# Optimization experiments

Measured on AMD Instinct MI355X. Metric: run time of the kernel, lower is better.

Reference implementation:

```python
import jax, jax.numpy as jnp
import numpy as np

H = 8        # num_heads
KNN = 16     # k nearest neighbors
D = 256      # input_dim
LN_EPS = 1e-5


def _make_params(key, D):
    ks = jax.random.split(key, 10)
    def lin(k, din, dout):
        k1, k2 = jax.random.split(k)
        lim = 1.0 / np.sqrt(din)
        W = jax.random.uniform(k1, (din, dout), jnp.float32, -lim, lim)
        b = jax.random.uniform(k2, (dout,), jnp.float32, -lim, lim)
        return W, b
    Wq, bq = lin(ks[0], D, D)
    Wk, bk = lin(ks[1], D, D)
    Wv, bv = lin(ks[2], D, D)
    Wo1, bo1 = lin(ks[3], D, D)
    ln_g = jnp.ones((D,), jnp.float32)
    ln_b = jnp.zeros((D,), jnp.float32)
    Wo2, bo2 = lin(ks[4], D, D)
    return dict(Wq=Wq, bq=bq, Wk=Wk, bk=bk, Wv=Wv, bv=bv,
                Wo1=Wo1, bo1=bo1, ln_g=ln_g, ln_b=ln_b, Wo2=Wo2, bo2=bo2)


def setup_inputs() -> dict:
    key = jax.random.key(0)
    k1, k2, k3, k4, k5 = jax.random.split(key, 5)
    B, N, M = 2, 2048, 4096
    inp = {
        "src": jax.random.normal(k1, (B, N, 3), jnp.float32),
        "tgt": jax.random.normal(k2, (B, M, 3), jnp.float32),
        "src_fea": jax.random.normal(k3, (B, N, D), jnp.float32),
        "tgt_fea": jax.random.normal(k4, (B, M, D), jnp.float32),
    }
    inp.update(_make_params(k5, D))
    return inp


def _cdist(x, y):
    # Euclidean distance [B,N,M], matching torch.cdist(p=2)
    x2 = jnp.sum(x * x, axis=-1, keepdims=True)          # [B,N,1]
    y2 = jnp.sum(y * y, axis=-1, keepdims=True)          # [B,M,1]
    sq = x2 + jnp.swapaxes(y2, -1, -2) - 2.0 * jnp.einsum('bnc,bmc->bnm', x, y)
    return jnp.sqrt(jnp.maximum(sq, 0.0))


def _layernorm(x, g, b):
    mu = jnp.mean(x, axis=-1, keepdims=True)
    var = jnp.mean((x - mu) ** 2, axis=-1, keepdims=True)
    return (x - mu) * jax.lax.rsqrt(var + LN_EPS) * g + b


def reference(src, tgt, src_fea, tgt_fea, Wq, bq, Wk, bk, Wv, bv,
              Wo1, bo1, ln_g, ln_b, Wo2, bo2):
    B, N, Dm = src_fea.shape
    M = tgt.shape[1]
    dk = Dm // H
    scale = dk ** (-0.5)

    # kNN mask: distances [B,N,M], topk smallest -> boolean mask
    dist = _cdist(src, tgt)
    _, knn_idx = jax.lax.top_k(-dist, KNN)               # [B,N,KNN]
    bi = jnp.arange(B)[:, None, None]
    ni = jnp.arange(N)[None, :, None]
    mask = jnp.zeros((B, N, M), bool).at[bi, ni, knn_idx].set(True)

    # projections -> [B,H,*,dk]
    Q = (src_fea @ Wq + bq).reshape(B, N, H, dk).transpose(0, 2, 1, 3)
    K = (tgt_fea @ Wk + bk).reshape(B, M, H, dk).transpose(0, 2, 1, 3)
    V = (tgt_fea @ Wv + bv).reshape(B, M, H, dk).transpose(0, 2, 1, 3)

    scores = jnp.einsum('bhnd,bhmd->bhnm', Q, K) * scale
    scores = jnp.where(mask[:, None], scores, -jnp.inf)
    attn = jax.nn.softmax(scores, axis=-1)               # [B,H,N,M]

    out = jnp.einsum('bhnm,bhmd->bhnd', attn, V)
    out = out.transpose(0, 2, 1, 3).reshape(B, N, Dm)

    x = out + src_fea
    h = jax.nn.relu(_layernorm(x @ Wo1 + bo1, ln_g, ln_b))
    updated = h @ Wo2 + bo2

    avg_attn = jnp.mean(attn, axis=1)                    # [B,N,M]
    return updated, avg_attn
```

## Files before the change

kernel.cpp:

```cpp
#include <hip/hip_runtime.h>
#include <math.h>

#define BB 2
#define NN 2048
#define MM 4096
#define DD 256
#define HH 8
#define DK 32
#define KNN 16

typedef __attribute__((ext_vector_type(8))) short short8;
typedef __attribute__((ext_vector_type(4))) float f32x4;
typedef unsigned long long u64;
typedef unsigned short u16;

static __device__ __forceinline__ u16 f2bf(float f) {
    union { float f; unsigned u; } v; v.f = f;
    unsigned r = v.u + 0x7FFF + ((v.u >> 16) & 1);
    return (u16)(r >> 16);
}
static __device__ __forceinline__ float bf2f(u16 u) {
    union { unsigned u; float f; } v; v.u = ((unsigned)u) << 16;
    return v.f;
}

__global__ __launch_bounds__(256)
void wtrans(const float* W0, const float* W1, const float* W2, const float* W3, const float* W4,
            u16* O0, u16* O1, u16* O2, u16* O3, u16* O4)
{
    __shared__ float tile[64][65];
    const int bid = blockIdx.x;
    const int m = bid >> 4, tl = bid & 15;
    const int tr = (tl >> 2) * 64, tc = (tl & 3) * 64;
    const float* W = m == 0 ? W0 : m == 1 ? W1 : m == 2 ? W2 : m == 3 ? W3 : W4;
    u16*        O = m == 0 ? O0 : m == 1 ? O1 : m == 2 ? O2 : m == 3 ? O3 : O4;
    const int c = threadIdx.x & 63, r4 = threadIdx.x >> 6;
    #pragma unroll
    for (int i = 0; i < 16; ++i) {
        const int r = (r4 << 4) + i;
        tile[r][c] = W[(size_t)(tr + r) * 256 + tc + c];
    }
    __syncthreads();
    #pragma unroll
    for (int i = 0; i < 16; ++i) {
        const int cc = (r4 << 4) + i;
        O[(size_t)(tc + cc) * 256 + tr + c] = f2bf(tile[c][cc]);
    }
}

static __device__ __forceinline__ void gemm64_body(
    const float* __restrict__ A, size_t row0, const u16* __restrict__ WT, int col0,
    u16* As, u16* Bs, int t, f32x4 acc[2][2])
{
    const int lane = t & 63, w = t >> 6;
    const int wr = (w >> 1) * 32, wc = (w & 1) * 32;
    for (int k0 = 0; k0 < 256; k0 += 64) {
        #pragma unroll
        for (int e = 0; e < 2; ++e) {
            const int flat = t + (e << 8);
            const int r = flat >> 3, kc = (flat & 7) << 3;
            const int off = ((r << 7) + (kc << 1)) ^ ((r & 7) << 4);
            const float* ap = A + (row0 + r) * 256 + k0 + kc;
            float4 a0 = *(const float4*)ap;
            float4 a1 = *(const float4*)(ap + 4);
            short8 s;
            s[0] = (short)f2bf(a0.x); s[1] = (short)f2bf(a0.y);
            s[2] = (short)f2bf(a0.z); s[3] = (short)f2bf(a0.w);
            s[4] = (short)f2bf(a1.x); s[5] = (short)f2bf(a1.y);
            s[6] = (short)f2bf(a1.z); s[7] = (short)f2bf(a1.w);
            *(short8*)((char*)As + off) = s;
            *(short8*)((char*)Bs + off) = *(const short8*)(WT + (size_t)(col0 + r) * 256 + k0 + kc);
        }
        __syncthreads();
        #pragma unroll
        for (int kk = 0; kk < 64; kk += 32) {
            const int kbo = (kk + ((lane >> 4) << 3)) << 1;
            short8 af[2], bfr[2];
            #pragma unroll
            for (int i = 0; i < 2; ++i) {
                const int ra = wr + (i << 4) + (lane & 15);
                af[i]  = *(const short8*)((const char*)As + (((ra << 7) + kbo) ^ ((ra & 7) << 4)));
                const int rb = wc + (i << 4) + (lane & 15);
                bfr[i] = *(const short8*)((const char*)Bs + (((rb << 7) + kbo) ^ ((rb & 7) << 4)));
            }
            #pragma unroll
            for (int mi = 0; mi < 2; ++mi)
                #pragma unroll
                for (int ni = 0; ni < 2; ++ni)
                    acc[mi][ni] = __builtin_amdgcn_mfma_f32_16x16x32_bf16(af[mi], bfr[ni], acc[mi][ni], 0, 0, 0);
        }
        __syncthreads();
    }
}

__global__ __launch_bounds__(256, 4)
void mega_kernel(const float* __restrict__ src, const float* __restrict__ tgt,
                 int* __restrict__ knn_idx,
                 const float* __restrict__ tgt_fea, const float* __restrict__ src_fea,
                 const u16* __restrict__ WTq, const u16* __restrict__ WTkv,
                 const float* __restrict__ bq, const float* __restrict__ bk,
                 const float* __restrict__ bv,
                 float* __restrict__ Qb, u16* __restrict__ Kbf, u16* __restrict__ Vbf,
                 float* __restrict__ avg)
{
    __shared__ u16 As[64 * 64];
    __shared__ u16 Bs[64 * 64];
    const int bid = blockIdx.x;
    const int t = threadIdx.x;
    const int lane = t & 63;
    const int lid = bid / 11;
    const int role = bid % 11;

    if (role < 4) {
        const int kb = lid * 4 + role;
        const int bn = (kb << 2) + (t >> 6);
        const int b = bn >> 11;
        const float* sp = src + (size_t)bn * 3;
        const float px = sp[0], py = sp[1], pz = sp[2];
        const float x2 = px * px + py * py + pz * pz;
        const float* tb = tgt + (size_t)b * MM * 3;
        unsigned key[64];
        #pragma unroll
        for (int j = 0; j < 64; ++j) {
            const int m = (j << 6) + lane;
            const float tx = tb[m * 3 + 0], ty = tb[m * 3 + 1], tz = tb[m * 3 + 2];
            const float y2 = tx * tx + ty * ty + tz * tz;
            const float dt = px * tx + py * ty + pz * tz;
            float d = (x2 + y2) - 2.0f * dt;
            d = d > 0.f ? d : 0.f;
            const unsigned q20 = (unsigned)fminf(d * 32768.0f, 1048575.0f);
            key[j] = (q20 << 12) | (unsigned)m;
        }
        unsigned last1 = 0;
        unsigned mykey = 0xFFFFFFFFu;
        for (int sel = 0; sel < 20; ++sel) {
            unsigned c0 = ~0u, c1 = ~0u, c2 = ~0u, c3 = ~0u;
            #pragma unroll
            for (int j = 0; j < 64; j += 4) {
                const unsigned u0 = key[j + 0] - last1; c0 = u0 < c0 ? u0 : c0;
                const unsigned u1 = key[j + 1] - last1; c1 = u1 < c1 ? u1 : c1;
                const unsigned u2 = key[j + 2] - last1; c2 = u2 < c2 ? u2 : c2;
                const unsigned u3 = key[j + 3] - last1; c3 = u3 < c3 ? u3 : c3;
            }
            unsigned best = c0 < c1 ? c0 : c1;
            const unsigned bst2 = c2 < c3 ? c2 : c3;
            best = best < bst2 ? best : bst2;
            #pragma unroll
            for (int s = 32; s; s >>= 1) {
                const unsigned o = __shfl_xor(best, s, 64);
                best = o < best ? o : best;
            }
            const unsigned winner = best + last1;
            if (lane == sel) mykey = winner;
            last1 = winner + 1;
        }
        const int midx = (int)(mykey & 0xFFFu);
        u64 ex = ~0ULL;
        if (lane < 20) {
            const float* tp = tb + (size_t)midx * 3;
            const double pxd = px, pyd = py, pzd = pz;
            const double tx = tp[0], ty = tp[1], tz = tp[2];
            const double x2d = pxd * pxd + pyd * pyd + pzd * pzd;
            const double y2d = tx * tx + ty * ty + tz * tz;
            const double dtd = pxd * tx + pyd * ty + pzd * tz;
            double dd = (x2d + y2d) - 2.0 * dtd;
            dd = dd > 0.0 ? dd : 0.0;
            ex = (((u64)__double_as_longlong(dd)) & ~0xFFFULL) | (u64)midx;
        }
        int rank = 0;
        #pragma unroll
        for (int i = 0; i < 20; ++i) {
            const u64 o = __shfl(ex, i, 64);
            rank += (o < ex) ? 1 : 0;
        }
        if (lane < 20 && rank < 16)
            knn_idx[(size_t)bn * KNN + rank] = midx;
        return;
    }

    if (role < 8) {
        const int kvb = lid * 4 + (role - 4);
        const size_t row0 = (size_t)(kvb >> 3) * 64;
        const int col0 = (kvb & 7) * 64;
        f32x4 acc[2][2] = {};
        gemm64_body(tgt_fea, row0, WTkv, col0, As, Bs, t, acc);
        const int w = t >> 6;
        const int wr = (w >> 1) * 32, wc = (w & 1) * 32;
        const bool isv = col0 >= 256;
        u16* ob = isv ? Vbf : Kbf;
        const float* bs = isv ? bv : bk;
        const int cb = (isv ? col0 - 256 : col0) + wc;
        const int cq = lane & 15, rq = (lane >> 4) << 2;
        #pragma unroll
        for (int ni = 0; ni < 2; ++ni) {
            const int c = cb + (ni << 4) + cq;
            const float bval = bs[c];
            #pragma unroll
            for (int mi = 0; mi < 2; ++mi) {
                const size_t r = row0 + wr + (mi << 4) + rq;
                #pragma unroll
                for (int e = 0; e < 4; ++e)
                    ob[(r + e) * 256 + c] = f2bf(acc[mi][ni][e] + bval);
            }
        }
        return;
    }

    if (role == 8) {
        const int qb = lid;
        const size_t row0 = (size_t)(qb >> 2) * 64;
        const int col0 = (qb & 3) * 64;
        f32x4 acc[2][2] = {};
        gemm64_body(src_fea, row0, WTq, col0, As, Bs, t, acc);
        const int w = t >> 6;
        const int wr = (w >> 1) * 32, wc = (w & 1) * 32;
        const int cq = lane & 15, rq = (lane >> 4) << 2;
        #pragma unroll
        for (int ni = 0; ni < 2; ++ni) {
            const int c = col0 + wc + (ni << 4) + cq;
            const float bval = bq[c];
            #pragma unroll
            for (int mi = 0; mi < 2; ++mi) {
                const size_t rbase = (row0 + wr + (mi << 4) + rq) * 256 + c;
                #pragma unroll
                for (int e = 0; e < 4; ++e)
                    Qb[rbase + (size_t)e * 256] = acc[mi][ni][e] + bval;
            }
        }
        return;
    }

    {
        const int zb = lid * 2 + (role - 9);
        f32x4 z = {0.f, 0.f, 0.f, 0.f};
        f32x4* pz = (f32x4*)avg;
        const int base = zb * 256 + t;
        #pragma unroll
        for (int i = 0; i < 32; ++i)
            pz[base + i * 131072] = z;
    }
}

__global__ __launch_bounds__(256)
void attn_kernel(const float* __restrict__ Q, const u16* __restrict__ Kb,
                 const u16* __restrict__ Vb, const int* __restrict__ knn_idx,
                 const float* __restrict__ src_fea,
                 u16* __restrict__ Xb, float* __restrict__ avg_attn)
{
    __shared__ float Kt[KNN][257];
    __shared__ float Vt[KNN][257];
    __shared__ float q[DD];
    __shared__ float sc[HH][KNN];
    __shared__ float pw[HH][KNN];
    __shared__ int   idx[KNN];
    const int bn = blockIdx.x;
    const int b  = bn >> 11;
    const int t  = threadIdx.x;
    if (t < KNN) idx[t] = knn_idx[(size_t)bn * KNN + t];
    q[t] = Q[(size_t)bn * DD + t];
    __syncthreads();
    {
        const int l32 = t & 31, rg = t >> 5;
        #pragma unroll
        for (int rr = 0; rr < 2; ++rr) {
            const int r = (rr << 3) + rg;
            const size_t rowoff = ((size_t)b * MM + idx[r]) * DD + (l32 << 3);
            const short8 kv = *(const short8*)(Kb + rowoff);
            const short8 vv = *(const short8*)(Vb + rowoff);
            #pragma unroll
            for (int e = 0; e < 8; ++e) {
                Kt[r][(l32 << 3) + e] = bf2f((u16)kv[e]);
                Vt[r][(l32 << 3) + e] = bf2f((u16)vv[e]);
            }
        }
    }
    __syncthreads();
    if (t < HH * KNN) {
        int h = t >> 4, k = t & 15;
        float s = 0.f;
        const float* qh = &q[h * DK];
        const float* kh = &Kt[k][h * DK];
        #pragma unroll
        for (int j = 0; j < DK; ++j) s = fmaf(qh[j], kh[j], s);
        sc[h][k] = s * 0.17677669529663688f;
    }
    __syncthreads();
    if (t < HH) {
        float mx = -1e30f;
        #pragma unroll
        for (int k = 0; k < KNN; ++k) mx = fmaxf(mx, sc[t][k]);
        float e[KNN]; float sum = 0.f;
        #pragma unroll
        for (int k = 0; k < KNN; ++k) { e[k] = expf(sc[t][k] - mx); sum += e[k]; }
        float inv = 1.0f / sum;
        #pragma unroll
        for (int k = 0; k < KNN; ++k) pw[t][k] = e[k] * inv;
    }
    __syncthreads();
    if (t < KNN) {
        float a = 0.f;
        #pragma unroll
        for (int h = 0; h < HH; ++h) a += pw[h][t];
        avg_attn[(size_t)bn * MM + idx[t]] = a * (1.0f / HH);
    }
    {
        int h = t >> 5;
        float acc = 0.f;
        #pragma unroll
        for (int k = 0; k < KNN; ++k) acc = fmaf(pw[h][k], Vt[k][t], acc);
        Xb[(size_t)bn * DD + t] = f2bf(acc + src_fea[(size_t)bn * DD + t]);
    }
}

template<int LN>
__global__ __launch_bounds__(256)
void gemm_row256(const u16* __restrict__ A, const u16* __restrict__ WT,
                 const float* __restrict__ bias,
                 const float* __restrict__ g, const float* __restrict__ bvec,
                 u16* __restrict__ outb, float* __restrict__ outf)
{
    __shared__ u16 As[64 * 64];
    __shared__ u16 Bs[256 * 64];
    const int t = threadIdx.x, lane = t & 63, w = t >> 6;
    const size_t row0 = (size_t)blockIdx.x * 64;
    f32x4 acc[4][4] = {};
    for (int k0 = 0; k0 < 256; k0 += 64) {
        #pragma unroll
        for (int e = 0; e < 2; ++e) {
            const int u = t + (e << 8);
            const int r = u >> 3, kc = (u & 7) << 3;
            const int off = ((r << 7) + (kc << 1)) ^ ((r & 7) << 4);
            *(short8*)((char*)As + off) = *(const short8*)(A + (row0 + r) * 256 + k0 + kc);
        }
        #pragma unroll
        for (int e = 0; e < 8; ++e) {
            const int u = t + (e << 8);
            const int r = u >> 3, kc = (u & 7) << 3;
            const int off = ((r << 7) + (kc << 1)) ^ ((r & 7) << 4);
            *(short8*)((char*)Bs + off) = *(const short8*)(WT + (size_t)r * 256 + k0 + kc);
        }
        __syncthreads();
        #pragma unroll
        for (int kk = 0; kk < 64; kk += 32) {
            const int kbo = (kk + ((lane >> 4) << 3)) << 1;
            short8 af[4], bfr[4];
            #pragma unroll
            for (int i = 0; i < 4; ++i) {
                const int ra = (i << 4) + (lane & 15);
                af[i]  = *(const short8*)((const char*)As + (((ra << 7) + kbo) ^ ((ra & 7) << 4)));
                const int rb = (w << 6) + (i << 4) + (lane & 15);
                bfr[i] = *(const short8*)((const char*)Bs + (((rb << 7) + kbo) ^ ((rb & 7) << 4)));
            }
            #pragma unroll
            for (int mi = 0; mi < 4; ++mi)
                #pragma unroll
                for (int ni = 0; ni < 4; ++ni)
                    acc[mi][ni] = __builtin_amdgcn_mfma_f32_16x16x32_bf16(af[mi], bfr[ni], acc[mi][ni], 0, 0, 0);
        }
        __syncthreads();
    }
    const int cq = lane & 15, rq = (lane >> 4) << 2;
    #pragma unroll
    for (int ni = 0; ni < 4; ++ni) {
        const float bval = bias[(w << 6) + (ni << 4) + cq];
        #pragma unroll
        for (int mi = 0; mi < 4; ++mi)
            #pragma unroll
            for (int e = 0; e < 4; ++e)
                acc[mi][ni][e] += bval;
    }
    if (LN) {
        float* ws1 = (float*)As;
        float* ws2 = ws1 + 256;
        float s1v[4][4], s2v[4][4];
        #pragma unroll
        for (int mi = 0; mi < 4; ++mi)
            #pragma unroll
            for (int e = 0; e < 4; ++e) {
                float s1 = 0.f, s2 = 0.f;
                #pragma unroll
                for (int ni = 0; ni < 4; ++ni) { const float y = acc[mi][ni][e]; s1 += y; s2 += y * y; }
                #pragma unroll
                for (int s = 8; s; s >>= 1) { s1 += __shfl_xor(s1, s, 64); s2 += __shfl_xor(s2, s, 64); }
                s1v[mi][e] = s1; s2v[mi][e] = s2;
            }
        if (cq == 0) {
            #pragma unroll
            for (int mi = 0; mi < 4; ++mi)
                #pragma unroll
                for (int e = 0; e < 4; ++e) {
                    const int r = (mi << 4) + rq + e;
                    ws1[(w << 6) + r] = s1v[mi][e];
                    ws2[(w << 6) + r] = s2v[mi][e];
                }
        }
        __syncthreads();
        float g4[4], b4[4];
        #pragma unroll
        for (int ni = 0; ni < 4; ++ni) {
            const int c = (w << 6) + (ni << 4) + cq;
            g4[ni] = g[c]; b4[ni] = bvec[c];
        }
        #pragma unroll
        for (int mi = 0; mi < 4; ++mi)
            #pragma unroll
            for (int e = 0; e < 4; ++e) {
                const int r = (mi << 4) + rq + e;
                const float s1 = ws1[r] + ws1[64 + r] + ws1[128 + r] + ws1[192 + r];
                const float s2 = ws2[r] + ws2[64 + r] + ws2[128 + r] + ws2[192 + r];
                const float mean = s1 * (1.0f / 256.0f);
                const float var = s2 * (1.0f / 256.0f) - mean * mean;
                const float rstd = 1.0f / sqrtf(var + 1e-5f);
                #pragma unroll
                for (int ni = 0; ni < 4; ++ni) {
                    const int c = (w << 6) + (ni << 4) + cq;
                    float y = (acc[mi][ni][e] - mean) * rstd * g4[ni] + b4[ni];
                    outb[(row0 + r) * 256 + c] = f2bf(fmaxf(y, 0.0f));
                }
            }
    } else {
        #pragma unroll
        for (int ni = 0; ni < 4; ++ni) {
            const int c = (w << 6) + (ni << 4) + cq;
            #pragma unroll
            for (int mi = 0; mi < 4; ++mi) {
                const size_t rbase = (row0 + (mi << 4) + rq) * 256 + c;
                #pragma unroll
                for (int e = 0; e < 4; ++e)
                    outf[rbase + (size_t)e * 256] = acc[mi][ni][e];
            }
        }
    }
}

extern "C" void kernel_launch(void* const* d_in, const int* in_sizes, int n_in,
                              void* d_out, int out_size, void* d_ws, size_t ws_size,
                              hipStream_t stream) {
    const float* src     = (const float*)d_in[0];
    const float* tgt     = (const float*)d_in[1];
    const float* src_fea = (const float*)d_in[2];
    const float* tgt_fea = (const float*)d_in[3];
    const float* Wq  = (const float*)d_in[4];   const float* bq  = (const float*)d_in[5];
    const float* Wk  = (const float*)d_in[6];   const float* bk  = (const float*)d_in[7];
    const float* Wv  = (const float*)d_in[8];   const float* bv  = (const float*)d_in[9];
    const float* Wo1 = (const float*)d_in[10];  const float* bo1 = (const float*)d_in[11];
    const float* lng = (const float*)d_in[12];  const float* lnb = (const float*)d_in[13];
    const float* Wo2 = (const float*)d_in[14];  const float* bo2 = (const float*)d_in[15];
    (void)in_sizes; (void)n_in; (void)out_size; (void)ws_size;

    float* out     = (float*)d_out;
    float* updated = out;
    float* avg     = out + (size_t)BB * NN * DD;

    char* p = (char*)d_ws;
    u16* WTq  = (u16*)p;   p += 256 * 256 * 2;
    u16* WTk  = (u16*)p;   p += 256 * 256 * 2;
    u16* WTv  = (u16*)p;   p += 256 * 256 * 2;
    u16* WTo1 = (u16*)p;   p += 256 * 256 * 2;
    u16* WTo2 = (u16*)p;   p += 256 * 256 * 2;
    float* Qb = (float*)p; p += (size_t)BB * NN * DD * 4;
    u16* Kbf  = (u16*)p;   p += (size_t)BB * MM * DD * 2;
    u16* Vbf  = (u16*)p;   p += (size_t)BB * MM * DD * 2;
    int* knn  = (int*)p;   p += (size_t)BB * NN * KNN * 4;
    u16* Xbf  = (u16*)p;   p += (size_t)BB * NN * DD * 2;
    u16* Hbf  = (u16*)p;   p += (size_t)BB * NN * DD * 2;

    dim3 blk(256);
    wtrans<<<80, blk, 0, stream>>>(Wq, Wk, Wv, Wo1, Wo2, WTq, WTk, WTv, WTo1, WTo2);
    mega_kernel<<<2816, blk, 0, stream>>>(src, tgt, knn, tgt_fea, src_fea, WTq, WTk,
                                          bq, bk, bv, Qb, Kbf, Vbf, avg);
    attn_kernel<<<BB * NN, blk, 0, stream>>>(Qb, Kbf, Vbf, knn, src_fea, Xbf, avg);
    gemm_row256<1><<<BB * NN / 64, blk, 0, stream>>>(Xbf, WTo1, bo1, lng, lnb, Hbf, nullptr);
    gemm_row256<0><<<BB * NN / 64, blk, 0, stream>>>(Hbf, WTo2, bo2, nullptr, nullptr, nullptr, updated);
}
```

Baseline: 201.5 us.

## Use one wave per query in attention and shrink output GEMM tiles for more blocks

The attention kernel now handles four queries per block, one wavefront each. Each wave computes the 16 neighbour scores straight from global bf16 K rows and runs the softmax and head-average reductions with wave shuffles, so the K/V staging into shared memory and most barriers go away. The two output GEMMs drop from 64-row tiles to 32-row tiles, and the Wo2 GEMM also splits columns across two blocks. This launches many more blocks to fill the GPU's CUs, at the cost of reloading the weight tiles more often.

```diff
diff --git a/kernel.cpp b/kernel.cpp
--- a/kernel.cpp
+++ b/kernel.cpp
@@ -10,6 +10,7 @@
 #define KNN 16
 
 typedef __attribute__((ext_vector_type(8))) short short8;
+typedef __attribute__((ext_vector_type(4))) short short4v;
 typedef __attribute__((ext_vector_type(4))) float f32x4;
 typedef unsigned long long u64;
 typedef unsigned short u16;
@@ -247,88 +248,100 @@
                  const float* __restrict__ src_fea,
                  u16* __restrict__ Xb, float* __restrict__ avg_attn)
 {
-    __shared__ float Kt[KNN][257];
-    __shared__ float Vt[KNN][257];
-    __shared__ float q[DD];
-    __shared__ float sc[HH][KNN];
-    __shared__ float pw[HH][KNN];
-    __shared__ int   idx[KNN];
-    const int bn = blockIdx.x;
-    const int b  = bn >> 11;
-    const int t  = threadIdx.x;
-    if (t < KNN) idx[t] = knn_idx[(size_t)bn * KNN + t];
-    q[t] = Q[(size_t)bn * DD + t];
+    __shared__ float q_sh[4][256];
+    __shared__ float pw_sh[4][8][17];
+    __shared__ int   idx_sh[4][16];
+    const int t = threadIdx.x;
+    const int wid = t >> 6, lane = t & 63;
+    const int bn = (blockIdx.x << 2) + wid;
+    const int b = bn >> 11;
+    const int h = lane >> 3, k2 = lane & 7;
+
+    *(float4*)&q_sh[wid][lane << 2] = *(const float4*)(Q + (size_t)bn * 256 + (lane << 2));
+    const int ia = knn_idx[(size_t)bn * KNN + k2];
+    const int ib = knn_idx[(size_t)bn * KNN + 8 + k2];
     __syncthreads();
-    {
-        const int l32 = t & 31, rg = t >> 5;
-        #pragma unroll
-        for (int rr = 0; rr < 2; ++rr) {
-            const int r = (rr << 3) + rg;
-            const size_t rowoff = ((size_t)b * MM + idx[r]) * DD + (l32 << 3);
-            const short8 kv = *(const short8*)(Kb + rowoff);
-            const short8 vv = *(const short8*)(Vb + rowoff);
-            #pragma unroll
-            for (int e = 0; e < 8; ++e) {
-                Kt[r][(l32 << 3) + e] = bf2f((u16)kv[e]);
-                Vt[r][(l32 << 3) + e] = bf2f((u16)vv[e]);
-            }
-        }
-    }
+
+    const u16* Ka = Kb + ((size_t)b * MM + ia) * 256 + h * DK;
+    const u16* Kc = Kb + ((size_t)b * MM + ib) * 256 + h * DK;
+    const float* qh = &q_sh[wid][h * DK];
+    float s0 = 0.f, s1 = 0.f;
+    #pragma unroll
+    for (int j = 0; j < DK; j += 8) {
+        const short8 ka = *(const short8*)(Ka + j);
+        const short8 kc = *(const short8*)(Kc + j);
+        #pragma unroll
+        for (int e = 0; e < 8; ++e) {
+            const float qv = qh[j + e];
+            s0 = fmaf(qv, bf2f((u16)ka[e]), s0);
+            s1 = fmaf(qv, bf2f((u16)kc[e]), s1);
+        }
+    }
+    s0 *= 0.17677669529663688f;
+    s1 *= 0.17677669529663688f;
+
+    float m = fmaxf(s0, s1);
+    m = fmaxf(m, __shfl_xor(m, 1, 64));
+    m = fmaxf(m, __shfl_xor(m, 2, 64));
+    m = fmaxf(m, __shfl_xor(m, 4, 64));
+    const float e0 = expf(s0 - m), e1 = expf(s1 - m);
+    float sum = e0 + e1;
+    sum += __shfl_xor(sum, 1, 64);
+    sum += __shfl_xor(sum, 2, 64);
+    sum += __shfl_xor(sum, 4, 64);
+    const float inv = 1.0f / sum;
+    const float p0 = e0 * inv, p1 = e1 * inv;
+
+    float a0 = p0, a1 = p1;
+    a0 += __shfl_xor(a0, 8, 64);  a1 += __shfl_xor(a1, 8, 64);
+    a0 += __shfl_xor(a0, 16, 64); a1 += __shfl_xor(a1, 16, 64);
+    a0 += __shfl_xor(a0, 32, 64); a1 += __shfl_xor(a1, 32, 64);
+    if (h == 0) {
+        avg_attn[(size_t)bn * MM + ia] = a0 * 0.125f;
+        avg_attn[(size_t)bn * MM + ib] = a1 * 0.125f;
+        idx_sh[wid][k2] = ia;
+        idx_sh[wid][8 + k2] = ib;
+    }
+    pw_sh[wid][h][k2] = p0;
+    pw_sh[wid][h][8 + k2] = p1;
     __syncthreads();
-    if (t < HH * KNN) {
-        int h = t >> 4, k = t & 15;
-        float s = 0.f;
-        const float* qh = &q[h * DK];
-        const float* kh = &Kt[k][h * DK];
-        #pragma unroll
-        for (int j = 0; j < DK; ++j) s = fmaf(qh[j], kh[j], s);
-        sc[h][k] = s * 0.17677669529663688f;
-    }
-    __syncthreads();
-    if (t < HH) {
-        float mx = -1e30f;
-        #pragma unroll
-        for (int k = 0; k < KNN; ++k) mx = fmaxf(mx, sc[t][k]);
-        float e[KNN]; float sum = 0.f;
-        #pragma unroll
-        for (int k = 0; k < KNN; ++k) { e[k] = expf(sc[t][k] - mx); sum += e[k]; }
-        float inv = 1.0f / sum;
-        #pragma unroll
-        for (int k = 0; k < KNN; ++k) pw[t][k] = e[k] * inv;
-    }
-    __syncthreads();
-    if (t < KNN) {
-        float a = 0.f;
-        #pragma unroll
-        for (int h = 0; h < HH; ++h) a += pw[h][t];
-        avg_attn[(size_t)bn * MM + idx[t]] = a * (1.0f / HH);
-    }
-    {
-        int h = t >> 5;
-        float acc = 0.f;
-        #pragma unroll
-        for (int k = 0; k < KNN; ++k) acc = fmaf(pw[h][k], Vt[k][t], acc);
-        Xb[(size_t)bn * DD + t] = f2bf(acc + src_fea[(size_t)bn * DD + t]);
-    }
-}
-
-template<int LN>
+
+    const int d0 = lane << 2;
+    const int h2 = lane >> 3;
+    float o0 = 0.f, o1 = 0.f, o2 = 0.f, o3 = 0.f;
+    #pragma unroll
+    for (int k = 0; k < KNN; ++k) {
+        const float p = pw_sh[wid][h2][k];
+        const int ik = idx_sh[wid][k];
+        const short4v v4 = *(const short4v*)(Vb + ((size_t)b * MM + ik) * 256 + d0);
+        o0 = fmaf(p, bf2f((u16)v4[0]), o0);
+        o1 = fmaf(p, bf2f((u16)v4[1]), o1);
+        o2 = fmaf(p, bf2f((u16)v4[2]), o2);
+        o3 = fmaf(p, bf2f((u16)v4[3]), o3);
+    }
+    const float4 sf = *(const float4*)(src_fea + (size_t)bn * 256 + d0);
+    short4v xo;
+    xo[0] = (short)f2bf(o0 + sf.x);
+    xo[1] = (short)f2bf(o1 + sf.y);
+    xo[2] = (short)f2bf(o2 + sf.z);
+    xo[3] = (short)f2bf(o3 + sf.w);
+    *(short4v*)(Xb + (size_t)bn * 256 + d0) = xo;
+}
+
 __global__ __launch_bounds__(256)
-void gemm_row256(const u16* __restrict__ A, const u16* __restrict__ WT,
+void gemm_wo1_ln(const u16* __restrict__ A, const u16* __restrict__ WT,
                  const float* __restrict__ bias,
                  const float* __restrict__ g, const float* __restrict__ bvec,
-                 u16* __restrict__ outb, float* __restrict__ outf)
+                 u16* __restrict__ outb)
 {
-    __shared__ u16 As[64 * 64];
+    __shared__ u16 As[32 * 64];
     __shared__ u16 Bs[256 * 64];
     const int t = threadIdx.x, lane = t & 63, w = t >> 6;
-    const size_t row0 = (size_t)blockIdx.x * 64;
-    f32x4 acc[4][4] = {};
+    const size_t row0 = (size_t)blockIdx.x * 32;
+    f32x4 acc[2][4] = {};
     for (int k0 = 0; k0 < 256; k0 += 64) {
-        #pragma unroll
-        for (int e = 0; e < 2; ++e) {
-            const int u = t + (e << 8);
-            const int r = u >> 3, kc = (u & 7) << 3;
+        {
+            const int r = t >> 3, kc = (t & 7) << 3;
             const int off = ((r << 7) + (kc << 1)) ^ ((r & 7) << 4);
             *(short8*)((char*)As + off) = *(const short8*)(A + (row0 + r) * 256 + k0 + kc);
         }
@@ -343,16 +356,19 @@
         #pragma unroll
         for (int kk = 0; kk < 64; kk += 32) {
             const int kbo = (kk + ((lane >> 4) << 3)) << 1;
-            short8 af[4], bfr[4];
+            short8 af[2], bfr[4];
+            #pragma unroll
+            for (int i = 0; i < 2; ++i) {
+                const int ra = (i << 4) + (lane & 15);
+                af[i] = *(const short8*)((const char*)As + (((ra << 7) + kbo) ^ ((ra & 7) << 4)));
+            }
             #pragma unroll
             for (int i = 0; i < 4; ++i) {
-                const int ra = (i << 4) + (lane & 15);
-                af[i]  = *(const short8*)((const char*)As + (((ra << 7) + kbo) ^ ((ra & 7) << 4)));
                 const int rb = (w << 6) + (i << 4) + (lane & 15);
                 bfr[i] = *(const short8*)((const char*)Bs + (((rb << 7) + kbo) ^ ((rb & 7) << 4)));
             }
             #pragma unroll
-            for (int mi = 0; mi < 4; ++mi)
+            for (int mi = 0; mi < 2; ++mi)
                 #pragma unroll
                 for (int ni = 0; ni < 4; ++ni)
                     acc[mi][ni] = __builtin_amdgcn_mfma_f32_16x16x32_bf16(af[mi], bfr[ni], acc[mi][ni], 0, 0, 0);
@@ -364,71 +380,110 @@
     for (int ni = 0; ni < 4; ++ni) {
         const float bval = bias[(w << 6) + (ni << 4) + cq];
         #pragma unroll
-        for (int mi = 0; mi < 4; ++mi)
+        for (int mi = 0; mi < 2; ++mi)
             #pragma unroll
             for (int e = 0; e < 4; ++e)
                 acc[mi][ni][e] += bval;
     }
-    if (LN) {
-        float* ws1 = (float*)As;
-        float* ws2 = ws1 + 256;
-        float s1v[4][4], s2v[4][4];
-        #pragma unroll
-        for (int mi = 0; mi < 4; ++mi)
-            #pragma unroll
-            for (int e = 0; e < 4; ++e) {
-                float s1 = 0.f, s2 = 0.f;
+    float* ws1 = (float*)As;
+    float* ws2 = ws1 + 128;
+    #pragma unroll
+    for (int mi = 0; mi < 2; ++mi)
+        #pragma unroll
+        for (int e = 0; e < 4; ++e) {
+            float s1 = 0.f, s2 = 0.f;
+            #pragma unroll
+            for (int ni = 0; ni < 4; ++ni) { const float y = acc[mi][ni][e]; s1 += y; s2 += y * y; }
+            s1 += __shfl_xor(s1, 1, 64); s2 += __shfl_xor(s2, 1, 64);
+            s1 += __shfl_xor(s1, 2, 64); s2 += __shfl_xor(s2, 2, 64);
+            s1 += __shfl_xor(s1, 4, 64); s2 += __shfl_xor(s2, 4, 64);
+            s1 += __shfl_xor(s1, 8, 64); s2 += __shfl_xor(s2, 8, 64);
+            if (cq == 0) {
+                const int r = (mi << 4) + rq + e;
+                ws1[(w << 5) + r] = s1;
+                ws2[(w << 5) + r] = s2;
+            }
+        }
+    __syncthreads();
+    float g4[4], b4[4];
+    #pragma unroll
+    for (int ni = 0; ni < 4; ++ni) {
+        const int c = (w << 6) + (ni << 4) + cq;
+        g4[ni] = g[c]; b4[ni] = bvec[c];
+    }
+    #pragma unroll
+    for (int mi = 0; mi < 2; ++mi)
+        #pragma unroll
+        for (int e = 0; e < 4; ++e) {
+            const int r = (mi << 4) + rq + e;
+            const float s1 = ws1[r] + ws1[32 + r] + ws1[64 + r] + ws1[96 + r];
+            const float s2 = ws2[r] + ws2[32 + r] + ws2[64 + r] + ws2[96 + r];
+            const float mean = s1 * (1.0f / 256.0f);
+            const float var = s2 * (1.0f / 256.0f) - mean * mean;
+            const float rstd = 1.0f / sqrtf(var + 1e-5f);
+            #pragma unroll
+            for (int ni = 0; ni < 4; ++ni) {
+                const int c = (w << 6) + (ni << 4) + cq;
+                const float y = (acc[mi][ni][e] - mean) * rstd * g4[ni] + b4[ni];
+                outb[(row0 + r) * 256 + c] = f2bf(fmaxf(y, 0.0f));
+            }
+        }
+}
+
+__global__ __launch_bounds__(256)
+void gemm_wo2(const u16* __restrict__ A, const u16* __restrict__ WT,
+              const float* __restrict__ bias, float* __restrict__ outf)
+{
+    __shared__ u16 As[32 * 64];
+    __shared__ u16 Bs[128 * 64];
+    const int t = threadIdx.x, lane = t & 63, w = t >> 6;
+    const size_t row0 = (size_t)(blockIdx.x >> 1) * 32;
+    const int col0 = (blockIdx.x & 1) * 128;
+    f32x4 acc[2][2] = {};
+    for (int k0 = 0; k0 < 256; k0 += 64) {
+        {
+            const int r = t >> 3, kc = (t & 7) << 3;
+            const int off = ((r << 7) + (kc << 1)) ^ ((r & 7) << 4);
+            *(short8*)((char*)As + off) = *(const short8*)(A + (row0 + r) * 256 + k0 + kc);
+        }
+        #pragma unroll
+        for (int e = 0; e < 4; ++e) {
+            const int u = t + (e << 8);
+            const int r = u >> 3, kc = (u & 7) << 3;
+            const int off = ((r << 7) + (kc << 1)) ^ ((r & 7) << 4);
+            *(short8*)((char*)Bs + off) = *(const short8*)(WT + (size_t)(col0 + r) * 256 + k0 + kc);
+        }
+        __syncthreads();
+        #pragma unroll
+        for (int kk = 0; kk < 64; kk += 32) {
+            const int kbo = (kk + ((lane >> 4) << 3)) << 1;
+            short8 af[2], bfr[2];
+            #pragma unroll
+            for (int i = 0; i < 2; ++i) {
+                const int ra = (i << 4) + (lane & 15);
+                af[i] = *(const short8*)((const char*)As + (((ra << 7) + kbo) ^ ((ra & 7) << 4)));
+                const int rb = (w << 5) + (i << 4) + (lane & 15);
+                bfr[i] = *(const short8*)((const char*)Bs + (((rb << 7) + kbo) ^ ((rb & 7) << 4)));
+            }
+            #pragma unroll
+            for (int mi = 0; mi < 2; ++mi)
                 #pragma unroll
-                for (int ni = 0; ni < 4; ++ni) { const float y = acc[mi][ni][e]; s1 += y; s2 += y * y; }
-                #pragma unroll
-                for (int s = 8; s; s >>= 1) { s1 += __shfl_xor(s1, s, 64); s2 += __shfl_xor(s2, s, 64); }
-                s1v[mi][e] = s1; s2v[mi][e] = s2;
-            }
-        if (cq == 0) {
-            #pragma unroll
-            for (int mi = 0; mi < 4; ++mi)
-                #pragma unroll
-                for (int e = 0; e < 4; ++e) {
-                    const int r = (mi << 4) + rq + e;
-                    ws1[(w << 6) + r] = s1v[mi][e];
-                    ws2[(w << 6) + r] = s2v[mi][e];
-                }
+                for (int ni = 0; ni < 2; ++ni)
+                    acc[mi][ni] = __builtin_amdgcn_mfma_f32_16x16x32_bf16(af[mi], bfr[ni], acc[mi][ni], 0, 0, 0);
         }
         __syncthreads();
-        float g4[4], b4[4];
-        #pragma unroll
-        for (int ni = 0; ni < 4; ++ni) {
-            const int c = (w << 6) + (ni << 4) + cq;
-            g4[ni] = g[c]; b4[ni] = bvec[c];
-        }
-        #pragma unroll
-        for (int mi = 0; mi < 4; ++mi)
-            #pragma unroll
-            for (int e = 0; e < 4; ++e) {
-                const int r = (mi << 4) + rq + e;
-                const float s1 = ws1[r] + ws1[64 + r] + ws1[128 + r] + ws1[192 + r];
-                const float s2 = ws2[r] + ws2[64 + r] + ws2[128 + r] + ws2[192 + r];
-                const float mean = s1 * (1.0f / 256.0f);
-                const float var = s2 * (1.0f / 256.0f) - mean * mean;
-                const float rstd = 1.0f / sqrtf(var + 1e-5f);
-                #pragma unroll
-                for (int ni = 0; ni < 4; ++ni) {
-                    const int c = (w << 6) + (ni << 4) + cq;
-                    float y = (acc[mi][ni][e] - mean) * rstd * g4[ni] + b4[ni];
-                    outb[(row0 + r) * 256 + c] = f2bf(fmaxf(y, 0.0f));
-                }
-            }
-    } else {
-        #pragma unroll
-        for (int ni = 0; ni < 4; ++ni) {
-            const int c = (w << 6) + (ni << 4) + cq;
-            #pragma unroll
-            for (int mi = 0; mi < 4; ++mi) {
-                const size_t rbase = (row0 + (mi << 4) + rq) * 256 + c;
-                #pragma unroll
-                for (int e = 0; e < 4; ++e)
-                    outf[rbase + (size_t)e * 256] = acc[mi][ni][e];
-            }
+    }
+    const int cq = lane & 15, rq = (lane >> 4) << 2;
+    #pragma unroll
+    for (int ni = 0; ni < 2; ++ni) {
+        const int c = col0 + (w << 5) + (ni << 4) + cq;
+        const float bval = bias[c];
+        #pragma unroll
+        for (int mi = 0; mi < 2; ++mi) {
+            const size_t rbase = (row0 + (mi << 4) + rq) * 256 + c;
+            #pragma unroll
+            for (int e = 0; e < 4; ++e)
+                outf[rbase + (size_t)e * 256] = acc[mi][ni][e] + bval;
         }
     }
 }
@@ -469,7 +524,7 @@
     wtrans<<<80, blk, 0, stream>>>(Wq, Wk, Wv, Wo1, Wo2, WTq, WTk, WTv, WTo1, WTo2);
     mega_kernel<<<2816, blk, 0, stream>>>(src, tgt, knn, tgt_fea, src_fea, WTq, WTk,
                                           bq, bk, bv, Qb, Kbf, Vbf, avg);
-    attn_kernel<<<BB * NN, blk, 0, stream>>>(Qb, Kbf, Vbf, knn, src_fea, Xbf, avg);
-    gemm_row256<1><<<BB * NN / 64, blk, 0, stream>>>(Xbf, WTo1, bo1, lng, lnb, Hbf, nullptr);
-    gemm_row256<0><<<BB * NN / 64, blk, 0, stream>>>(Hbf, WTo2, bo2, nullptr, nullptr, nullptr, updated);
-}
+    attn_kernel<<<BB * NN / 4, blk, 0, stream>>>(Qb, Kbf, Vbf, knn, src_fea, Xbf, avg);
+    gemm_wo1_ln<<<BB * NN / 32, blk, 0, stream>>>(Xbf, WTo1, bo1, lng, lnb, Hbf);
+    gemm_wo2<<<BB * NN / 16, blk, 0, stream>>>(Hbf, WTo2, bo2, updated);
+}
```

Result: faster. 183.7 us (-8.8%).
